# Kernel tuning notes

Hardware: AMD Instinct MI355X
Metric: run time of the kernel (lower is better)

Reference implementation:

```python
import jax, jax.numpy as jnp
import numpy as np

DEPTH = 4
EPS = 1e-5


def block_pool(x, g):
    # adaptive max pool over a g x g grid of blocks, broadcast back to full size.
    # Equivalent to the recursive HalfSplit/adaptive_max_pool2d/QuarterStitch pyramid.
    B, C, H, W = x.shape
    xr = x.reshape(B, C, g, H // g, g, W // g)
    m = xr.max(axis=(3, 5), keepdims=True)          # [B,C,g,1,g,1]
    return jnp.broadcast_to(m, xr.shape).reshape(B, C, H, W)


def conv1x1_bn(x, w, gamma, beta):
    # Conv2DNormed: 1x1 conv (no bias) followed by BatchNorm (batch statistics).
    y = jnp.einsum('bchw,oc->bohw', x, w)
    mu = y.mean(axis=(0, 2, 3), keepdims=True)
    var = y.var(axis=(0, 2, 3), keepdims=True)
    yhat = (y - mu) * jax.lax.rsqrt(var + EPS)
    return yhat * gamma[None, :, None, None] + beta[None, :, None, None]


def setup_inputs() -> dict:
    key = jax.random.key(0)
    k0, k1, k2 = jax.random.split(key, 3)
    B, C, H, W = 4, 256, 192, 192
    x = jax.random.normal(k0, (B, C, H, W), jnp.float32)
    ws = jax.random.normal(k1, (DEPTH, C, C), jnp.float32) / np.float32(np.sqrt(C))
    gs = jnp.ones((DEPTH, C), jnp.float32)
    bs = jnp.zeros((DEPTH, C), jnp.float32)
    wf = jax.random.normal(k2, (C, (DEPTH + 1) * C), jnp.float32) / np.float32(np.sqrt((DEPTH + 1) * C))
    gf = jnp.ones((C,), jnp.float32)
    bf = jnp.zeros((C,), jnp.float32)
    return {"x": x, "ws": ws, "gs": gs, "bs": bs, "wf": wf, "gf": gf, "bf": bf}


def reference(x, ws, gs, bs, wf, gf, bf):
    # p[0] = raw input; p[1+d] = conv_d(block-pooled input at grid 2^d), d=0..DEPTH-1
    p = [x]
    for d in range(DEPTH):
        pooled = block_pool(x, 2 ** d)
        p.append(conv1x1_bn(pooled, ws[d], gs[d], bs[d]))
    out = jnp.concatenate(p, axis=1)                # [B, (DEPTH+1)*C, H, W]
    return conv1x1_bn(out, wf, gf, bf)
```

## Files before the change

### kernel.cpp

```cpp
#include <hip/hip_runtime.h>

typedef unsigned short u16;
typedef unsigned int   u32;
typedef __attribute__((ext_vector_type(4))) float f32x4;
typedef __attribute__((ext_vector_type(8))) short s16x8;
typedef __attribute__((ext_vector_type(4))) unsigned short u16x4;
typedef __attribute__((ext_vector_type(8))) unsigned short u16x8;

#define HW    36864
#define NCH   256
#define NB    4
#define NPIX  147456
#define POS   85
#define BN_EPS 1e-5f
#define NBKT  16

#define WS_PALL    0
#define WS_YD      87040
#define WS_PSUM    174080
#define WS_PSQ     175104
#define WS_CONTRIB 176128
#define WS_FSUMB   241664
#define WS_FSQB    245760
#define WS_WPK     249856
#define WS_YBF     282624
#define WS_TOT1    (WS_YBF + NB*NCH*HW/2)

__device__ __forceinline__ u16 f2bf(float f) {
  u32 u = __builtin_bit_cast(u32, f);
  u += 0x7fffu + ((u >> 16) & 1u);
  return (u16)(u >> 16);
}
__device__ __forceinline__ float bf2f(u16 h) {
  u32 u = ((u32)h) << 16;
  return __builtin_bit_cast(float, u);
}

__global__ __launch_bounds__(192) void k_pool(const float* __restrict__ x,
                                              const float* __restrict__ wf,
                                              float* __restrict__ wsb) {
  int blk = blockIdx.x;
  int t = threadIdx.x;
  if (blk >= 1024) {
    int fid = (blk - 1024)*192 + t;
    if (fid < 8192) {
      int m = fid & 255, g = (fid >> 8) & 3, ks = fid >> 10;
      const float* src = wf + (size_t)m*1280 + ks*32 + g*8;
      f32x4 a = *(const f32x4*)src;
      f32x4 c = *(const f32x4*)(src + 4);
      u32* dst = (u32*)((u16*)(wsb + WS_WPK) + (size_t)fid*8);
      dst[0] = (u32)f2bf(a.x) | ((u32)f2bf(a.y) << 16);
      dst[1] = (u32)f2bf(a.z) | ((u32)f2bf(a.w) << 16);
      dst[2] = (u32)f2bf(c.x) | ((u32)f2bf(c.y) << 16);
      dst[3] = (u32)f2bf(c.z) | ((u32)f2bf(c.w) << 16);
    }
    return;
  }
  __shared__ float sm[8][4][48];
  __shared__ float sp[84];
  int bc = blk;
  const float* base = x + (size_t)bc * HW;
  int cg = t % 48, rg = t / 48;
  if (bc == 0) {
    for (int i = t; i < 2048; i += 192) wsb[WS_PSUM + i] = 0.f;
    for (int i = t; i < 8192; i += 192) wsb[WS_FSUMB + i] = 0.f;
    for (int i = t; i < 65536; i += 192) wsb[WS_CONTRIB + i] = 0.f;
  }
  #pragma unroll
  for (int byi = 0; byi < 8; byi++) {
    float mm = -3.4e38f;
    #pragma unroll
    for (int rr = 0; rr < 6; rr++) {
      int r = byi*24 + rg + 4*rr;
      f32x4 v = *(const f32x4*)(base + r*192 + cg*4);
      mm = fmaxf(mm, fmaxf(fmaxf(v.x, v.y), fmaxf(v.z, v.w)));
    }
    sm[byi][rg][cg] = mm;
  }
  __syncthreads();
  size_t pb = WS_PALL + (size_t)bc * POS;
  if (t < 64) {
    int by = t >> 3, bx = t & 7;
    float mm = -3.4e38f;
    for (int r2 = 0; r2 < 4; r2++)
      for (int cq = 0; cq < 6; cq++)
        mm = fmaxf(mm, sm[by][r2][bx*6 + cq]);
    sp[t] = mm;
    wsb[pb + t] = mm;
  }
  __syncthreads();
  if (t < 16) {
    int i = t >> 2, j = t & 3;
    float mm = fmaxf(fmaxf(sp[(2*i)*8 + 2*j], sp[(2*i)*8 + 2*j + 1]),
                     fmaxf(sp[(2*i+1)*8 + 2*j], sp[(2*i+1)*8 + 2*j + 1]));
    sp[64 + t] = mm;
    wsb[pb + 64 + t] = mm;
  }
  __syncthreads();
  if (t < 4) {
    int i = t >> 1, j = t & 1;
    float mm = fmaxf(fmaxf(sp[64 + (2*i)*4 + 2*j], sp[64 + (2*i)*4 + 2*j + 1]),
                     fmaxf(sp[64 + (2*i+1)*4 + 2*j], sp[64 + (2*i+1)*4 + 2*j + 1]));
    sp[80 + t] = mm;
    wsb[pb + 80 + t] = mm;
  }
  __syncthreads();
  if (t == 0)
    wsb[pb + 84] = fmaxf(fmaxf(sp[80], sp[81]), fmaxf(sp[82], sp[83]));
}

__global__ __launch_bounds__(256) void k_pyr(const float* __restrict__ wconv, float* __restrict__ wsb) {
  __shared__ __align__(16) float pv[256];
  int bi = blockIdx.x;
  int b = bi / 85, pos = bi % 85;
  int d = (pos < 64) ? 3 : (pos < 80) ? 2 : (pos < 84) ? 1 : 0;
  int t = threadIdx.x;
  pv[t] = wsb[WS_PALL + (size_t)(b*NCH + t)*POS + pos];
  __syncthreads();
  const float* wrow = wconv + ((size_t)d*NCH + t)*NCH;
  float acc = 0.f;
  #pragma unroll 4
  for (int c4 = 0; c4 < 64; c4++) {
    f32x4 wv = *(const f32x4*)(wrow + c4*4);
    f32x4 xv = *(const f32x4*)(&pv[c4*4]);
    acc += wv.x*xv.x + wv.y*xv.y + wv.z*xv.z + wv.w*xv.w;
  }
  wsb[WS_YD + (size_t)(b*NCH + t)*POS + pos] = acc;
  atomicAdd(&wsb[WS_PSUM + d*NCH + t], acc);
  atomicAdd(&wsb[WS_PSQ  + d*NCH + t], acc*acc);
}

__global__ __launch_bounds__(256) void k_contrib(const float* __restrict__ wf,
                                                 const float* __restrict__ gs,
                                                 const float* __restrict__ bs,
                                                 float* __restrict__ wsb) {
  __shared__ __align__(16) float pn[4][256];
  int bi = blockIdx.x;
  int d = bi >> 6, cell = bi & 63;
  int by = cell >> 3, bx = cell & 7;
  int t = threadIdx.x;
  int pos = (d == 3) ? cell
          : (d == 2) ? 64 + (by >> 1)*4 + (bx >> 1)
          : (d == 1) ? 80 + (by >> 2)*2 + (bx >> 2)
          : 84;
  float cnt = (float)(4 << (2*d));
  float mu  = wsb[WS_PSUM + d*NCH + t] / cnt;
  float var = wsb[WS_PSQ  + d*NCH + t] / cnt - mu*mu;
  float sc  = gs[d*NCH + t] * rsqrtf(var + BN_EPS);
  float bi_ = bs[d*NCH + t] - mu * sc;
  #pragma unroll
  for (int b = 0; b < 4; b++)
    pn[b][t] = wsb[WS_YD + (size_t)(b*NCH + t)*POS + pos] * sc + bi_;
  __syncthreads();
  const float* wrow = wf + (size_t)t*1280 + 256 + d*256;
  float a0 = 0.f, a1 = 0.f, a2 = 0.f, a3 = 0.f;
  #pragma unroll 4
  for (int j = 0; j < 64; j++) {
    f32x4 wv = *(const f32x4*)(wrow + j*4);
    f32x4 p0 = *(const f32x4*)(&pn[0][j*4]);
    f32x4 p1 = *(const f32x4*)(&pn[1][j*4]);
    f32x4 p2 = *(const f32x4*)(&pn[2][j*4]);
    f32x4 p3 = *(const f32x4*)(&pn[3][j*4]);
    a0 += wv.x*p0.x + wv.y*p0.y + wv.z*p0.z + wv.w*p0.w;
    a1 += wv.x*p1.x + wv.y*p1.y + wv.z*p1.z + wv.w*p1.w;
    a2 += wv.x*p2.x + wv.y*p2.y + wv.z*p2.z + wv.w*p2.w;
    a3 += wv.x*p3.x + wv.y*p3.y + wv.z*p3.z + wv.w*p3.w;
  }
  atomicAdd(&wsb[WS_CONTRIB + (size_t)(0*NCH + t)*64 + cell], a0);
  atomicAdd(&wsb[WS_CONTRIB + (size_t)(1*NCH + t)*64 + cell], a1);
  atomicAdd(&wsb[WS_CONTRIB + (size_t)(2*NCH + t)*64 + cell], a2);
  atomicAdd(&wsb[WS_CONTRIB + (size_t)(3*NCH + t)*64 + cell], a3);
}

template<bool YBF>
__global__ __launch_bounds__(256, 3) void k_main(const float* __restrict__ x,
                                                 float* __restrict__ wsb, float* __restrict__ y) {
  __shared__ __align__(16) char smem[40960];
  __shared__ float ctile[256*4];
  u32* xbuf = (u32*)smem;
  int wg = blockIdx.x;
  int b = wg / 576, tile = wg % 576;
  int n0 = tile * 64;
  int t = threadIdx.x, w = t >> 6, l = t & 63, g = l >> 4, ln = l & 15;
  int cb0 = (tile % 3) * 64;
  int rowblk = (tile / 3) / 24;
  int cblk0 = cb0 / 24;
  const u16* wpk = (const u16*)(wsb + WS_WPK);
  int mrow = w*64 + ln;
  int qq = t & 15, c2 = t >> 4;
  const float* xsrc = x + (size_t)(b*NCH + 2*c2)*HW + n0 + 4*qq;

  float ct[4];
  {
    const float* cbase = wsb + WS_CONTRIB + ((size_t)b*NCH + t)*64 + rowblk*8;
    #pragma unroll
    for (int i = 0; i < 4; i++) {
      int cc = cblk0 + i; if (cc > 7) cc = 7;
      ct[i] = cbase[cc];
    }
  }
  f32x4 xr[2][2][2];
  #pragma unroll
  for (int pp = 0; pp < 2; pp++)
    #pragma unroll
    for (int s = 0; s < 2; s++)
      #pragma unroll
      for (int h = 0; h < 2; h++)
        xr[pp][s][h] = *(const f32x4*)(xsrc + (size_t)((pp*2 + s)*32 + h)*HW);

  #pragma unroll
  for (int i = 0; i < 4; i++) ctile[t*4 + i] = ct[i];
  asm volatile("s_waitcnt lgkmcnt(0)" ::: "memory");
  __builtin_amdgcn_s_barrier();

  f32x4 acc[4][4];
  #pragma unroll
  for (int i = 0; i < 4; i++)
    #pragma unroll
    for (int j = 0; j < 4; j++)
      acc[i][j] = {0.f, 0.f, 0.f, 0.f};

  int slot = (((c2 >> 2) ^ (qq & 3)) << 2) | (c2 & 3);

  #pragma unroll
  for (int p = 0; p < 4; p++) {
    {
      u32* dst = xbuf + (p & 1)*2560;
      #pragma unroll
      for (int s = 0; s < 2; s++) {
        f32x4 va = xr[p & 1][s][0], vb = xr[p & 1][s][1];
        #pragma unroll
        for (int j = 0; j < 4; j++) {
          u32 pk = (u32)f2bf(va[j]) | ((u32)f2bf(vb[j]) << 16);
          dst[(4*qq + j)*40 + s*20 + slot] = pk;
        }
      }
    }
    asm volatile("s_waitcnt lgkmcnt(0)" ::: "memory");
    __builtin_amdgcn_s_barrier();
    if (p < 2) {
      #pragma unroll
      for (int s = 0; s < 2; s++)
        #pragma unroll
        for (int h = 0; h < 2; h++)
          xr[p & 1][s][h] = *(const f32x4*)(xsrc + (size_t)(((p+2)*2 + s)*32 + h)*HW);
    }
    #pragma unroll
    for (int s = 0; s < 2; s++) {
      int sl = p*2 + s;
      s16x8 af[4];
      #pragma unroll
      for (int tm = 0; tm < 4; tm++)
        af[tm] = *(const s16x8*)(wpk + ((size_t)(sl*4 + g)*256 + mrow + tm*16)*8);
      const u32* xb = xbuf + (p & 1)*2560 + s*20;
      #pragma unroll
      for (int tn = 0; tn < 4; tn++) {
        int px = 16*tn + ln;
        int gr = g ^ ((px >> 2) & 3);
        s16x8 bfr = *(const s16x8*)((const u16*)&xb[px*40 + gr*4]);
        #pragma unroll
        for (int tm = 0; tm < 4; tm++)
          acc[tm][tn] = __builtin_amdgcn_mfma_f32_16x16x32_bf16(af[tm], bfr, acc[tm][tn], 0, 0, 0);
      }
    }
  }

  __syncthreads();
  u16* ytile = (u16*)smem;
  int ci[4];
  #pragma unroll
  for (int tn = 0; tn < 4; tn++)
    ci[tn] = (cb0 + 16*tn + ln)/24 - cblk0;
  int bkt = wg & (NBKT - 1);
  float* fsum = wsb + WS_FSUMB + bkt*256;
  float* fsq  = wsb + WS_FSQB  + bkt*256;
  float* yf   = y + (size_t)b*NCH*HW + n0;
  #pragma unroll
  for (int tm = 0; tm < 4; tm++) {
    #pragma unroll
    for (int r = 0; r < 4; r++) {
      int o = w*64 + tm*16 + g*4 + r;
      float s1 = 0.f, s2 = 0.f;
      #pragma unroll
      for (int tn = 0; tn < 4; tn++) {
        int px = 16*tn + ln;
        float v = acc[tm][tn][r] + ctile[o*4 + ci[tn]];
        if (YBF) {
          u16 h = f2bf(v);
          ytile[o*72 + px] = h;
          float yr = bf2f(h);
          s1 += yr; s2 += yr*yr;
        } else {
          yf[(size_t)o*HW + px] = v;
          s1 += v; s2 += v*v;
        }
      }
      s1 += __shfl_xor(s1, 1);  s2 += __shfl_xor(s2, 1);
      s1 += __shfl_xor(s1, 2);  s2 += __shfl_xor(s2, 2);
      s1 += __shfl_xor(s1, 4);  s2 += __shfl_xor(s2, 4);
      s1 += __shfl_xor(s1, 8);  s2 += __shfl_xor(s2, 8);
      if (ln == 0) { atomicAdd(&fsum[o], s1); atomicAdd(&fsq[o], s2); }
    }
  }
  if (YBF) {
    __syncthreads();
    u16* ybb = (u16*)(wsb + WS_YBF) + (size_t)b*NCH*HW + n0;
    int oo = t >> 3, seg = t & 7;
    #pragma unroll
    for (int r8 = 0; r8 < 8; r8++) {
      int o = r8*32 + oo;
      u16x8 v = *(const u16x8*)(&ytile[o*72 + seg*8]);
      *(u16x8*)(ybb + (size_t)o*HW + seg*8) = v;
    }
  }
}

template<bool YBF>
__global__ __launch_bounds__(256) void k_norm(float* __restrict__ out,
                                              const float* __restrict__ gf,
                                              const float* __restrict__ bfv,
                                              const float* __restrict__ wsb) {
  int bid = blockIdx.x;
  int plane = bid >> 2, q = bid & 3;
  int c = plane & 255;
  float s1 = 0.f, s2 = 0.f;
  #pragma unroll
  for (int i = 0; i < NBKT; i++) {
    s1 += wsb[WS_FSUMB + i*256 + c];
    s2 += wsb[WS_FSQB  + i*256 + c];
  }
  float inv = 1.f / (float)NPIX;
  float mu  = s1 * inv;
  float var = s2 * inv - mu*mu;
  float sc  = gf[c] * rsqrtf(var + BN_EPS);
  float bi  = bfv[c] - mu * sc;
  size_t base4 = ((size_t)plane*HW + q*(HW/4)) >> 2;
  int t = threadIdx.x;
  if (YBF) {
    const u16* yb = (const u16*)(wsb + WS_YBF);
    #pragma unroll
    for (int it = 0; it < 9; it++) {
      size_t i4 = base4 + it*256 + t;
      u16x4 v = *(const u16x4*)(yb + i4*4);
      f32x4 o;
      o.x = bf2f(v[0])*sc + bi;
      o.y = bf2f(v[1])*sc + bi;
      o.z = bf2f(v[2])*sc + bi;
      o.w = bf2f(v[3])*sc + bi;
      ((f32x4*)out)[i4] = o;
    }
  } else {
    #pragma unroll
    for (int it = 0; it < 9; it++) {
      size_t i4 = base4 + it*256 + t;
      f32x4 v = ((f32x4*)out)[i4];
      v.x = v.x*sc + bi; v.y = v.y*sc + bi; v.z = v.z*sc + bi; v.w = v.w*sc + bi;
      ((f32x4*)out)[i4] = v;
    }
  }
}

extern "C" void kernel_launch(void* const* d_in, const int* in_sizes, int n_in,
                              void* d_out, int out_size, void* d_ws, size_t ws_size,
                              hipStream_t stream) {
  const float* x  = (const float*)d_in[0];
  const float* w  = (const float*)d_in[1];
  const float* gs = (const float*)d_in[2];
  const float* bs = (const float*)d_in[3];
  const float* wf = (const float*)d_in[4];
  const float* gf = (const float*)d_in[5];
  const float* bf = (const float*)d_in[6];
  float* y   = (float*)d_out;
  float* wsb = (float*)d_ws;

  bool ybf = ws_size >= (size_t)WS_TOT1 * sizeof(float);

  k_pool   <<<1068, 192, 0, stream>>>(x, wf, wsb);
  k_pyr    <<<NB*POS, 256, 0, stream>>>(w, wsb);
  k_contrib<<<256, 256, 0, stream>>>(wf, gs, bs, wsb);
  if (ybf) k_main<true> <<<NB*576, 256, 0, stream>>>(x, wsb, y);
  else     k_main<false><<<NB*576, 256, 0, stream>>>(x, wsb, y);
  if (ybf) k_norm<true> <<<4096, 256, 0, stream>>>(y, gf, bf, wsb);
  else     k_norm<false><<<4096, 256, 0, stream>>>(y, gf, bf, wsb);
}
```

Measured before the change: 176.9 us.

## Fuse block max-pooling into main GEMM and defer pyramid contribution to normalization

The separate pooling pass over x is removed. k_main now computes per-tile partial block maxima while staging x, so x is read from HBM once instead of twice. Because the pyramid contribution is no longer added inside the GEMM, the main kernel stores raw partial per-cell sums and sum-of-squares per tile. A new k_fstats kernel combines these with the contribution term analytically to get the BN statistics, and k_norm applies a per-cell additive term. This brings extra kernels, a large per-tile partials workspace, and a larger bf16 workspace requirement that could disable the fast path.

```diff
diff --git a/kernel.cpp b/kernel.cpp
--- a/kernel.cpp
+++ b/kernel.cpp
@@ -13,18 +13,19 @@
 #define NPIX  147456
 #define POS   85
 #define BN_EPS 1e-5f
-#define NBKT  16
 
 #define WS_PALL    0
 #define WS_YD      87040
 #define WS_PSUM    174080
 #define WS_PSQ     175104
 #define WS_CONTRIB 176128
-#define WS_FSUMB   241664
-#define WS_FSQB    245760
-#define WS_WPK     249856
-#define WS_YBF     282624
-#define WS_TOT1    (WS_YBF + NB*NCH*HW/2)
+#define WS_SC      241664
+#define WS_ADD     241920
+#define WS_WPK     307456
+#define WS_PMP     340224
+#define WS_S1P     2699520
+#define WS_YBF     7418112
+#define WS_TOT1    26292480
 
 __device__ __forceinline__ u16 f2bf(float f) {
   u32 u = __builtin_bit_cast(u32, f);
@@ -36,77 +37,244 @@
   return __builtin_bit_cast(float, u);
 }
 
-__global__ __launch_bounds__(192) void k_pool(const float* __restrict__ x,
-                                              const float* __restrict__ wf,
-                                              float* __restrict__ wsb) {
-  int blk = blockIdx.x;
+__global__ __launch_bounds__(256) void k_prep(const float* __restrict__ wf, float* __restrict__ wsb) {
+  int blk = blockIdx.x, t = threadIdx.x;
+  if (blk < 32) {
+    int fid = blk*256 + t;
+    int m = fid & 255, g = (fid >> 8) & 3, ks = fid >> 10;
+    const float* src = wf + (size_t)m*1280 + ks*32 + g*8;
+    f32x4 a = *(const f32x4*)src;
+    f32x4 c = *(const f32x4*)(src + 4);
+    u32* dst = (u32*)((u16*)(wsb + WS_WPK) + (size_t)fid*8);
+    dst[0] = (u32)f2bf(a.x) | ((u32)f2bf(a.y) << 16);
+    dst[1] = (u32)f2bf(a.z) | ((u32)f2bf(a.w) << 16);
+    dst[2] = (u32)f2bf(c.x) | ((u32)f2bf(c.y) << 16);
+    dst[3] = (u32)f2bf(c.z) | ((u32)f2bf(c.w) << 16);
+    return;
+  }
+  int id = (blk - 32)*256 + t;
+  if (id < 65536) wsb[WS_CONTRIB + id] = 0.f;
+  else { int j = id - 65536; if (j < 2048) wsb[WS_PSUM + j] = 0.f; }
+}
+
+template<bool YBF>
+__global__ __launch_bounds__(256, 3) void k_main(const float* __restrict__ x,
+                                                 float* __restrict__ wsb, float* __restrict__ y) {
+  __shared__ __align__(16) char smem[40960];
+  u32* xbuf = (u32*)smem;
+  int wg = blockIdx.x;
+  int b = wg / 576, tile = wg % 576;
+  int n0 = tile * 64;
+  int t = threadIdx.x, w = t >> 6, l = t & 63, g = l >> 4, ln = l & 15;
+  int cb0 = (tile % 3) * 64;
+  int cblk0 = cb0 / 24;
+  int maxcl = (cb0 + 63)/24 - cblk0;
+  const u16* wpk = (const u16*)(wsb + WS_WPK);
+  int mrow = w*64 + ln;
+  int qq = t & 15, c2 = t >> 4;
+  const float* xsrc = x + (size_t)(b*NCH + 2*c2)*HW + n0 + 4*qq;
+
+  f32x4 xr[2][2][2];
+  #pragma unroll
+  for (int pp = 0; pp < 2; pp++)
+    #pragma unroll
+    for (int s = 0; s < 2; s++)
+      #pragma unroll
+      for (int h = 0; h < 2; h++)
+        xr[pp][s][h] = *(const f32x4*)(xsrc + (size_t)((pp*2 + s)*32 + h)*HW);
+
+  f32x4 acc[4][4];
+  #pragma unroll
+  for (int i = 0; i < 4; i++)
+    #pragma unroll
+    for (int j = 0; j < 4; j++)
+      acc[i][j] = {0.f, 0.f, 0.f, 0.f};
+
+  float pmA[8], pmB[8];
+  int slot = (((c2 >> 2) ^ (qq & 3)) << 2) | (c2 & 3);
+
+  #pragma unroll
+  for (int p = 0; p < 4; p++) {
+    {
+      u32* dst = xbuf + (p & 1)*2560;
+      #pragma unroll
+      for (int s = 0; s < 2; s++) {
+        f32x4 va = xr[p & 1][s][0], vb = xr[p & 1][s][1];
+        #pragma unroll
+        for (int j = 0; j < 4; j++) {
+          u32 pk = (u32)f2bf(va[j]) | ((u32)f2bf(vb[j]) << 16);
+          dst[(4*qq + j)*40 + s*20 + slot] = pk;
+        }
+        pmA[p*2 + s] = fmaxf(fmaxf(va.x, va.y), fmaxf(va.z, va.w));
+        pmB[p*2 + s] = fmaxf(fmaxf(vb.x, vb.y), fmaxf(vb.z, vb.w));
+      }
+    }
+    asm volatile("s_waitcnt lgkmcnt(0)" ::: "memory");
+    __builtin_amdgcn_s_barrier();
+    if (p < 2) {
+      #pragma unroll
+      for (int s = 0; s < 2; s++)
+        #pragma unroll
+        for (int h = 0; h < 2; h++)
+          xr[p & 1][s][h] = *(const f32x4*)(xsrc + (size_t)(((p+2)*2 + s)*32 + h)*HW);
+    }
+    #pragma unroll
+    for (int s = 0; s < 2; s++) {
+      int sl = p*2 + s;
+      s16x8 af[4];
+      #pragma unroll
+      for (int tm = 0; tm < 4; tm++)
+        af[tm] = *(const s16x8*)(wpk + ((size_t)(sl*4 + g)*256 + mrow + tm*16)*8);
+      const u32* xb = xbuf + (p & 1)*2560 + s*20;
+      #pragma unroll
+      for (int tn = 0; tn < 4; tn++) {
+        int px = 16*tn + ln;
+        int gr = g ^ ((px >> 2) & 3);
+        s16x8 bfr = *(const s16x8*)((const u16*)&xb[px*40 + gr*4]);
+        #pragma unroll
+        for (int tm = 0; tm < 4; tm++)
+          acc[tm][tn] = __builtin_amdgcn_mfma_f32_16x16x32_bf16(af[tm], bfr, acc[tm][tn], 0, 0, 0);
+      }
+    }
+  }
+
+  __syncthreads();
+  float* pml = (float*)smem;
+  #pragma unroll
+  for (int sl = 0; sl < 8; sl++) {
+    pml[(sl*32 + 2*c2)*17 + qq]     = pmA[sl];
+    pml[(sl*32 + 2*c2 + 1)*17 + qq] = pmB[sl];
+  }
+  __syncthreads();
+  {
+    float m0 = -3.4e38f, m1 = -3.4e38f, m2 = -3.4e38f, m3 = -3.4e38f;
+    #pragma unroll
+    for (int q = 0; q < 16; q++) {
+      float v = pml[t*17 + q];
+      int cl = (cb0 + 4*q)/24 - cblk0;
+      m0 = (cl == 0) ? fmaxf(m0, v) : m0;
+      m1 = (cl == 1) ? fmaxf(m1, v) : m1;
+      m2 = (cl == 2) ? fmaxf(m2, v) : m2;
+      m3 = (cl == 3) ? fmaxf(m3, v) : m3;
+    }
+    float* pmp = wsb + WS_PMP + (((size_t)b*NCH + t)*576 + tile)*4;
+    pmp[0] = m0;
+    if (1 <= maxcl) pmp[1] = m1;
+    if (2 <= maxcl) pmp[2] = m2;
+    if (3 <= maxcl) pmp[3] = m3;
+  }
+  __syncthreads();
+
+  float* s1p = wsb + WS_S1P + (((size_t)b*576 + tile)*256)*8;
+
+  if (YBF) {
+    u16* ytile = (u16*)smem;
+    #pragma unroll
+    for (int tm = 0; tm < 4; tm++)
+      #pragma unroll
+      for (int r = 0; r < 4; r++) {
+        int orow = w*64 + tm*16 + g*4 + r;
+        #pragma unroll
+        for (int tn = 0; tn < 4; tn++)
+          ytile[orow*72 + 16*tn + ln] = f2bf(acc[tm][tn][r]);
+      }
+    __syncthreads();
+    int seg = t & 7, oo = t >> 3;
+    int lbase = l & 56;
+    int cl_s = (cb0 + 8*seg)/24 - cblk0;
+    int nx1 = (seg < 7) ? ((cb0 + 8*(seg+1))/24 - cblk0) : 99;
+    int nx2 = (seg < 6) ? ((cb0 + 8*(seg+2))/24 - cblk0) : 99;
+    bool i1 = (nx1 == cl_s), i2 = (nx2 == cl_s);
+    bool ist = (seg == 0) || (((cb0 + 8*seg) % 24) == 0);
+    u16* ybb = (u16*)(wsb + WS_YBF) + (size_t)b*NCH*HW + n0;
+    #pragma unroll
+    for (int r8i = 0; r8i < 8; r8i++) {
+      int o = r8i*32 + oo;
+      u16x8 v = *(const u16x8*)(&ytile[o*72 + seg*8]);
+      *(u16x8*)(ybb + (size_t)o*HW + seg*8) = v;
+      float sval = 0.f, sq = 0.f;
+      #pragma unroll
+      for (int e = 0; e < 8; e++) { float yr = bf2f(v[e]); sval += yr; sq += yr*yr; }
+      float s2t = sq;
+      s2t += __shfl_xor(s2t, 1); s2t += __shfl_xor(s2t, 2); s2t += __shfl_xor(s2t, 4);
+      float v1 = __shfl(sval, lbase + ((seg + 1) & 7));
+      float v2 = __shfl(sval, lbase + ((seg + 2) & 7));
+      float cell = sval + (i1 ? v1 : 0.f) + (i2 ? v2 : 0.f);
+      if (ist) s1p[(size_t)o*8 + cl_s] = cell;
+      if (seg == 0) s1p[(size_t)o*8 + 4] = s2t;
+    }
+  } else {
+    float* yf = y + (size_t)b*NCH*HW + n0;
+    int ci_[4];
+    #pragma unroll
+    for (int tn = 0; tn < 4; tn++) ci_[tn] = (cb0 + 16*tn + ln)/24 - cblk0;
+    #pragma unroll
+    for (int tm = 0; tm < 4; tm++)
+      #pragma unroll
+      for (int r = 0; r < 4; r++) {
+        int o = w*64 + tm*16 + g*4 + r;
+        float sv0 = 0.f, sv1 = 0.f, sv2 = 0.f, sv3 = 0.f, s2 = 0.f;
+        #pragma unroll
+        for (int tn = 0; tn < 4; tn++) {
+          int px = 16*tn + ln;
+          float v = acc[tm][tn][r];
+          yf[(size_t)o*HW + px] = v;
+          s2 += v*v;
+          sv0 += (ci_[tn] == 0) ? v : 0.f;
+          sv1 += (ci_[tn] == 1) ? v : 0.f;
+          sv2 += (ci_[tn] == 2) ? v : 0.f;
+          sv3 += (ci_[tn] == 3) ? v : 0.f;
+        }
+        #pragma unroll
+        for (int off = 1; off < 16; off <<= 1) {
+          sv0 += __shfl_xor(sv0, off); sv1 += __shfl_xor(sv1, off);
+          sv2 += __shfl_xor(sv2, off); sv3 += __shfl_xor(sv3, off);
+          s2  += __shfl_xor(s2, off);
+        }
+        if (ln < 4) {
+          float out = (ln == 0) ? sv0 : (ln == 1) ? sv1 : (ln == 2) ? sv2 : sv3;
+          s1p[(size_t)o*8 + ln] = out;
+        }
+        if (ln == 0) s1p[(size_t)o*8 + 4] = s2;
+      }
+  }
+}
+
+__global__ __launch_bounds__(64) void k_pred(float* __restrict__ wsb) {
+  __shared__ float sm3[64], sm2[16], sm1[4];
+  int bc = blockIdx.x;
   int t = threadIdx.x;
-  if (blk >= 1024) {
-    int fid = (blk - 1024)*192 + t;
-    if (fid < 8192) {
-      int m = fid & 255, g = (fid >> 8) & 3, ks = fid >> 10;
-      const float* src = wf + (size_t)m*1280 + ks*32 + g*8;
-      f32x4 a = *(const f32x4*)src;
-      f32x4 c = *(const f32x4*)(src + 4);
-      u32* dst = (u32*)((u16*)(wsb + WS_WPK) + (size_t)fid*8);
-      dst[0] = (u32)f2bf(a.x) | ((u32)f2bf(a.y) << 16);
-      dst[1] = (u32)f2bf(a.z) | ((u32)f2bf(a.w) << 16);
-      dst[2] = (u32)f2bf(c.x) | ((u32)f2bf(c.y) << 16);
-      dst[3] = (u32)f2bf(c.z) | ((u32)f2bf(c.w) << 16);
-    }
-    return;
-  }
-  __shared__ float sm[8][4][48];
-  __shared__ float sp[84];
-  int bc = blk;
-  const float* base = x + (size_t)bc * HW;
-  int cg = t % 48, rg = t / 48;
-  if (bc == 0) {
-    for (int i = t; i < 2048; i += 192) wsb[WS_PSUM + i] = 0.f;
-    for (int i = t; i < 8192; i += 192) wsb[WS_FSUMB + i] = 0.f;
-    for (int i = t; i < 65536; i += 192) wsb[WS_CONTRIB + i] = 0.f;
-  }
-  #pragma unroll
-  for (int byi = 0; byi < 8; byi++) {
-    float mm = -3.4e38f;
-    #pragma unroll
-    for (int rr = 0; rr < 6; rr++) {
-      int r = byi*24 + rg + 4*rr;
-      f32x4 v = *(const f32x4*)(base + r*192 + cg*4);
-      mm = fmaxf(mm, fmaxf(fmaxf(v.x, v.y), fmaxf(v.z, v.w)));
-    }
-    sm[byi][rg][cg] = mm;
-  }
-  __syncthreads();
-  size_t pb = WS_PALL + (size_t)bc * POS;
-  if (t < 64) {
-    int by = t >> 3, bx = t & 7;
-    float mm = -3.4e38f;
-    for (int r2 = 0; r2 < 4; r2++)
-      for (int cq = 0; cq < 6; cq++)
-        mm = fmaxf(mm, sm[by][r2][bx*6 + cq]);
-    sp[t] = mm;
-    wsb[pb + t] = mm;
-  }
-  __syncthreads();
+  int by = t >> 3, bx = t & 7;
+  const float* pmp = wsb + WS_PMP + (size_t)bc*576*4;
+  int tc0 = (24*bx)/64, tc1 = (24*bx + 23)/64;
+  float m = -3.4e38f;
+  for (int r = 0; r < 24; r++) {
+    int row = by*24 + r;
+    for (int tc = tc0; tc <= tc1; tc++) {
+      int cblk0 = (tc*64)/24;
+      m = fmaxf(m, pmp[(size_t)(row*3 + tc)*4 + (bx - cblk0)]);
+    }
+  }
+  sm3[t] = m;
+  __syncthreads();
+  float* pb = wsb + WS_PALL + (size_t)bc*POS;
+  pb[t] = m;
   if (t < 16) {
     int i = t >> 2, j = t & 3;
-    float mm = fmaxf(fmaxf(sp[(2*i)*8 + 2*j], sp[(2*i)*8 + 2*j + 1]),
-                     fmaxf(sp[(2*i+1)*8 + 2*j], sp[(2*i+1)*8 + 2*j + 1]));
-    sp[64 + t] = mm;
-    wsb[pb + 64 + t] = mm;
+    float mm = fmaxf(fmaxf(sm3[(2*i)*8 + 2*j], sm3[(2*i)*8 + 2*j + 1]),
+                     fmaxf(sm3[(2*i+1)*8 + 2*j], sm3[(2*i+1)*8 + 2*j + 1]));
+    sm2[t] = mm; pb[64 + t] = mm;
   }
   __syncthreads();
   if (t < 4) {
     int i = t >> 1, j = t & 1;
-    float mm = fmaxf(fmaxf(sp[64 + (2*i)*4 + 2*j], sp[64 + (2*i)*4 + 2*j + 1]),
-                     fmaxf(sp[64 + (2*i+1)*4 + 2*j], sp[64 + (2*i+1)*4 + 2*j + 1]));
-    sp[80 + t] = mm;
-    wsb[pb + 80 + t] = mm;
+    float mm = fmaxf(fmaxf(sm2[(2*i)*4 + 2*j], sm2[(2*i)*4 + 2*j + 1]),
+                     fmaxf(sm2[(2*i+1)*4 + 2*j], sm2[(2*i+1)*4 + 2*j + 1]));
+    sm1[t] = mm; pb[80 + t] = mm;
   }
   __syncthreads();
   if (t == 0)
-    wsb[pb + 84] = fmaxf(fmaxf(sp[80], sp[81]), fmaxf(sp[82], sp[83]));
+    pb[84] = fmaxf(fmaxf(sm1[0], sm1[1]), fmaxf(sm1[2], sm1[3]));
 }
 
 __global__ __launch_bounds__(256) void k_pyr(const float* __restrict__ wconv, float* __restrict__ wsb) {
@@ -172,189 +340,102 @@
   atomicAdd(&wsb[WS_CONTRIB + (size_t)(3*NCH + t)*64 + cell], a3);
 }
 
-template<bool YBF>
-__global__ __launch_bounds__(256, 3) void k_main(const float* __restrict__ x,
-                                                 float* __restrict__ wsb, float* __restrict__ y) {
-  __shared__ __align__(16) char smem[40960];
-  __shared__ float ctile[256*4];
-  u32* xbuf = (u32*)smem;
-  int wg = blockIdx.x;
-  int b = wg / 576, tile = wg % 576;
-  int n0 = tile * 64;
-  int t = threadIdx.x, w = t >> 6, l = t & 63, g = l >> 4, ln = l & 15;
-  int cb0 = (tile % 3) * 64;
-  int rowblk = (tile / 3) / 24;
-  int cblk0 = cb0 / 24;
-  const u16* wpk = (const u16*)(wsb + WS_WPK);
-  int mrow = w*64 + ln;
-  int qq = t & 15, c2 = t >> 4;
-  const float* xsrc = x + (size_t)(b*NCH + 2*c2)*HW + n0 + 4*qq;
-
-  float ct[4];
-  {
-    const float* cbase = wsb + WS_CONTRIB + ((size_t)b*NCH + t)*64 + rowblk*8;
-    #pragma unroll
-    for (int i = 0; i < 4; i++) {
-      int cc = cblk0 + i; if (cc > 7) cc = 7;
-      ct[i] = cbase[cc];
-    }
-  }
-  f32x4 xr[2][2][2];
-  #pragma unroll
-  for (int pp = 0; pp < 2; pp++)
-    #pragma unroll
-    for (int s = 0; s < 2; s++)
-      #pragma unroll
-      for (int h = 0; h < 2; h++)
-        xr[pp][s][h] = *(const f32x4*)(xsrc + (size_t)((pp*2 + s)*32 + h)*HW);
-
-  #pragma unroll
-  for (int i = 0; i < 4; i++) ctile[t*4 + i] = ct[i];
-  asm volatile("s_waitcnt lgkmcnt(0)" ::: "memory");
-  __builtin_amdgcn_s_barrier();
-
-  f32x4 acc[4][4];
-  #pragma unroll
-  for (int i = 0; i < 4; i++)
-    #pragma unroll
-    for (int j = 0; j < 4; j++)
-      acc[i][j] = {0.f, 0.f, 0.f, 0.f};
-
-  int slot = (((c2 >> 2) ^ (qq & 3)) << 2) | (c2 & 3);
-
-  #pragma unroll
-  for (int p = 0; p < 4; p++) {
-    {
-      u32* dst = xbuf + (p & 1)*2560;
-      #pragma unroll
-      for (int s = 0; s < 2; s++) {
-        f32x4 va = xr[p & 1][s][0], vb = xr[p & 1][s][1];
-        #pragma unroll
-        for (int j = 0; j < 4; j++) {
-          u32 pk = (u32)f2bf(va[j]) | ((u32)f2bf(vb[j]) << 16);
-          dst[(4*qq + j)*40 + s*20 + slot] = pk;
-        }
-      }
-    }
-    asm volatile("s_waitcnt lgkmcnt(0)" ::: "memory");
-    __builtin_amdgcn_s_barrier();
-    if (p < 2) {
-      #pragma unroll
-      for (int s = 0; s < 2; s++)
-        #pragma unroll
-        for (int h = 0; h < 2; h++)
-          xr[p & 1][s][h] = *(const f32x4*)(xsrc + (size_t)(((p+2)*2 + s)*32 + h)*HW);
-    }
-    #pragma unroll
-    for (int s = 0; s < 2; s++) {
-      int sl = p*2 + s;
-      s16x8 af[4];
-      #pragma unroll
-      for (int tm = 0; tm < 4; tm++)
-        af[tm] = *(const s16x8*)(wpk + ((size_t)(sl*4 + g)*256 + mrow + tm*16)*8);
-      const u32* xb = xbuf + (p & 1)*2560 + s*20;
-      #pragma unroll
-      for (int tn = 0; tn < 4; tn++) {
-        int px = 16*tn + ln;
-        int gr = g ^ ((px >> 2) & 3);
-        s16x8 bfr = *(const s16x8*)((const u16*)&xb[px*40 + gr*4]);
-        #pragma unroll
-        for (int tm = 0; tm < 4; tm++)
-          acc[tm][tn] = __builtin_amdgcn_mfma_f32_16x16x32_bf16(af[tm], bfr, acc[tm][tn], 0, 0, 0);
-      }
-    }
-  }
-
-  __syncthreads();
-  u16* ytile = (u16*)smem;
-  int ci[4];
-  #pragma unroll
-  for (int tn = 0; tn < 4; tn++)
-    ci[tn] = (cb0 + 16*tn + ln)/24 - cblk0;
-  int bkt = wg & (NBKT - 1);
-  float* fsum = wsb + WS_FSUMB + bkt*256;
-  float* fsq  = wsb + WS_FSQB  + bkt*256;
-  float* yf   = y + (size_t)b*NCH*HW + n0;
-  #pragma unroll
-  for (int tm = 0; tm < 4; tm++) {
-    #pragma unroll
-    for (int r = 0; r < 4; r++) {
-      int o = w*64 + tm*16 + g*4 + r;
-      float s1 = 0.f, s2 = 0.f;
-      #pragma unroll
-      for (int tn = 0; tn < 4; tn++) {
-        int px = 16*tn + ln;
-        float v = acc[tm][tn][r] + ctile[o*4 + ci[tn]];
-        if (YBF) {
-          u16 h = f2bf(v);
-          ytile[o*72 + px] = h;
-          float yr = bf2f(h);
-          s1 += yr; s2 += yr*yr;
-        } else {
-          yf[(size_t)o*HW + px] = v;
-          s1 += v; s2 += v*v;
-        }
-      }
-      s1 += __shfl_xor(s1, 1);  s2 += __shfl_xor(s2, 1);
-      s1 += __shfl_xor(s1, 2);  s2 += __shfl_xor(s2, 2);
-      s1 += __shfl_xor(s1, 4);  s2 += __shfl_xor(s2, 4);
-      s1 += __shfl_xor(s1, 8);  s2 += __shfl_xor(s2, 8);
-      if (ln == 0) { atomicAdd(&fsum[o], s1); atomicAdd(&fsq[o], s2); }
-    }
-  }
-  if (YBF) {
-    __syncthreads();
-    u16* ybb = (u16*)(wsb + WS_YBF) + (size_t)b*NCH*HW + n0;
-    int oo = t >> 3, seg = t & 7;
-    #pragma unroll
-    for (int r8 = 0; r8 < 8; r8++) {
-      int o = r8*32 + oo;
-      u16x8 v = *(const u16x8*)(&ytile[o*72 + seg*8]);
-      *(u16x8*)(ybb + (size_t)o*HW + seg*8) = v;
-    }
-  }
+__global__ __launch_bounds__(256) void k_fstats(const float* __restrict__ gf,
+                                                const float* __restrict__ bfv,
+                                                float* __restrict__ wsb) {
+  __shared__ float cs1[4][64];
+  __shared__ float red[12];
+  int o = blockIdx.x, t = threadIdx.x;
+  cs1[t >> 6][t & 63] = 0.f;
+  __syncthreads();
+  float sq = 0.f;
+  for (int e = t; e < 9216; e += 256) {
+    int slotv = e & 3, bt = e >> 2;
+    int tile = bt % 576, b = bt / 576;
+    int tm3 = tile % 3;
+    int mcl = (tm3 == 1) ? 3 : 2;
+    if (slotv <= mcl) {
+      float v = wsb[WS_S1P + (((size_t)b*576 + tile)*256 + o)*8 + slotv];
+      int cblk0 = (tm3 == 0) ? 0 : (tm3 == 1) ? 2 : 5;
+      int cell = ((tile/3)/24)*8 + cblk0 + slotv;
+      atomicAdd(&cs1[b][cell], v);
+    }
+  }
+  for (int e = t; e < 2304; e += 256) {
+    int tile = e % 576, b = e / 576;
+    sq += wsb[WS_S1P + (((size_t)b*576 + tile)*256 + o)*8 + 4];
+  }
+  __syncthreads();
+  int b4 = t >> 6, cell4 = t & 63;
+  float C  = wsb[WS_CONTRIB + ((size_t)(b4*NCH + o))*64 + cell4];
+  float s1 = cs1[b4][cell4];
+  float p1 = s1 + 576.f*C;
+  float p2 = C*(2.f*s1 + 576.f*C);
+  #pragma unroll
+  for (int off = 1; off < 64; off <<= 1) {
+    p1 += __shfl_xor(p1, off);
+    p2 += __shfl_xor(p2, off);
+    sq += __shfl_xor(sq, off);
+  }
+  int wv = t >> 6;
+  if ((t & 63) == 0) { red[wv] = p1; red[4 + wv] = p2; red[8 + wv] = sq; }
+  __syncthreads();
+  if (t == 0) {
+    float sum1 = red[0] + red[1] + red[2] + red[3];
+    float sum2 = red[4] + red[5] + red[6] + red[7]
+               + red[8] + red[9] + red[10] + red[11];
+    float inv = 1.f / (float)NPIX;
+    float mu  = sum1 * inv;
+    float var = sum2 * inv - mu*mu;
+    float sc  = gf[o] * rsqrtf(var + BN_EPS);
+    float bi  = bfv[o] - mu * sc;
+    wsb[WS_SC + o] = sc;
+    red[0] = sc; red[1] = bi;
+  }
+  __syncthreads();
+  float sc = red[0], bi = red[1];
+  wsb[WS_ADD + ((size_t)(b4*NCH + o))*64 + cell4] = bi + C*sc;
 }
 
 template<bool YBF>
 __global__ __launch_bounds__(256) void k_norm(float* __restrict__ out,
-                                              const float* __restrict__ gf,
-                                              const float* __restrict__ bfv,
                                               const float* __restrict__ wsb) {
+  __shared__ float a16[16];
   int bid = blockIdx.x;
   int plane = bid >> 2, q = bid & 3;
-  int c = plane & 255;
-  float s1 = 0.f, s2 = 0.f;
-  #pragma unroll
-  for (int i = 0; i < NBKT; i++) {
-    s1 += wsb[WS_FSUMB + i*256 + c];
-    s2 += wsb[WS_FSQB  + i*256 + c];
-  }
-  float inv = 1.f / (float)NPIX;
-  float mu  = s1 * inv;
-  float var = s2 * inv - mu*mu;
-  float sc  = gf[c] * rsqrtf(var + BN_EPS);
-  float bi  = bfv[c] - mu * sc;
+  int t = threadIdx.x;
+  float sc = wsb[WS_SC + (plane & 255)];
+  if (t < 16)
+    a16[t] = wsb[WS_ADD + (size_t)plane*64 + (2*q + (t >> 3))*8 + (t & 7)];
+  __syncthreads();
   size_t base4 = ((size_t)plane*HW + q*(HW/4)) >> 2;
-  int t = threadIdx.x;
   if (YBF) {
     const u16* yb = (const u16*)(wsb + WS_YBF);
     #pragma unroll
     for (int it = 0; it < 9; it++) {
+      int pl = 4*(it*256 + t);
+      int rl = pl / 192;
+      int cc = (pl - rl*192) / 24;
+      float ad = a16[(rl/24)*8 + cc];
       size_t i4 = base4 + it*256 + t;
       u16x4 v = *(const u16x4*)(yb + i4*4);
       f32x4 o;
-      o.x = bf2f(v[0])*sc + bi;
-      o.y = bf2f(v[1])*sc + bi;
-      o.z = bf2f(v[2])*sc + bi;
-      o.w = bf2f(v[3])*sc + bi;
+      o.x = bf2f(v[0])*sc + ad;
+      o.y = bf2f(v[1])*sc + ad;
+      o.z = bf2f(v[2])*sc + ad;
+      o.w = bf2f(v[3])*sc + ad;
       ((f32x4*)out)[i4] = o;
     }
   } else {
     #pragma unroll
     for (int it = 0; it < 9; it++) {
+      int pl = 4*(it*256 + t);
+      int rl = pl / 192;
+      int cc = (pl - rl*192) / 24;
+      float ad = a16[(rl/24)*8 + cc];
       size_t i4 = base4 + it*256 + t;
       f32x4 v = ((f32x4*)out)[i4];
-      v.x = v.x*sc + bi; v.y = v.y*sc + bi; v.z = v.z*sc + bi; v.w = v.w*sc + bi;
+      v.x = v.x*sc + ad; v.y = v.y*sc + ad; v.z = v.z*sc + ad; v.w = v.w*sc + ad;
       ((f32x4*)out)[i4] = v;
     }
   }
@@ -375,11 +456,13 @@
 
   bool ybf = ws_size >= (size_t)WS_TOT1 * sizeof(float);
 
-  k_pool   <<<1068, 192, 0, stream>>>(x, wf, wsb);
+  k_prep   <<<296, 256, 0, stream>>>(wf, wsb);
+  if (ybf) k_main<true> <<<NB*576, 256, 0, stream>>>(x, wsb, y);
+  else     k_main<false><<<NB*576, 256, 0, stream>>>(x, wsb, y);
+  k_pred   <<<NB*NCH, 64, 0, stream>>>(wsb);
   k_pyr    <<<NB*POS, 256, 0, stream>>>(w, wsb);
   k_contrib<<<256, 256, 0, stream>>>(wf, gs, bs, wsb);
-  if (ybf) k_main<true> <<<NB*576, 256, 0, stream>>>(x, wsb, y);
-  else     k_main<false><<<NB*576, 256, 0, stream>>>(x, wsb, y);
-  if (ybf) k_norm<true> <<<4096, 256, 0, stream>>>(y, gf, bf, wsb);
-  else     k_norm<false><<<4096, 256, 0, stream>>>(y, gf, bf, wsb);
-}
+  k_fstats <<<256, 256, 0, stream>>>(gf, bf, wsb);
+  if (ybf) k_norm<true> <<<4096, 256, 0, stream>>>(y, wsb);
+  else     k_norm<false><<<4096, 256, 0, stream>>>(y, wsb);
+}
```

New measurement: 207.4 us. 1.17x slower.
